# Kernel tuning notes

Measured on AMD Instinct MI355X. Metric: run time of the kernel, lower is better.

Reference implementation:

```python
import jax, jax.numpy as jnp
import numpy as np

L, V, D, H, F, S = 6, 32000, 768, 12, 3072, 1024
B, T = 2, 1024
DK = D // H
EPS = 1e-5  # torch LayerNorm default


def _ln(x, w, b):
    m = x.mean(-1, keepdims=True)
    v = ((x - m) ** 2).mean(-1, keepdims=True)
    return (x - m) / jnp.sqrt(v + EPS) * w + b


def setup_inputs() -> dict:
    key = jax.random.key(0)
    ks = jax.random.split(key, 16)
    n = lambda k, shape: jax.random.normal(k, shape, jnp.float32) * 0.02
    return {
        "x": jax.random.randint(ks[0], (B, T), 0, V),
        "tok_emb": n(ks[1], (V, D)),
        "pos_emb": n(ks[2], (S, D)),
        "ln1_w": jnp.ones((L, D), jnp.float32), "ln1_b": jnp.zeros((L, D), jnp.float32),
        "wq": n(ks[3], (L, D, D)), "bq": jnp.zeros((L, D), jnp.float32),
        "wk": n(ks[4], (L, D, D)), "bk": jnp.zeros((L, D), jnp.float32),
        "wv": n(ks[5], (L, D, D)), "bv": jnp.zeros((L, D), jnp.float32),
        "wo": n(ks[6], (L, D, D)), "bo": jnp.zeros((L, D), jnp.float32),
        "ln2_w": jnp.ones((L, D), jnp.float32), "ln2_b": jnp.zeros((L, D), jnp.float32),
        "w1": n(ks[7], (L, F, D)), "b1": jnp.zeros((L, F), jnp.float32),
        "w2": n(ks[8], (L, D, F)), "b2": jnp.zeros((L, D), jnp.float32),
        "lnf_w": jnp.ones((D,), jnp.float32), "lnf_b": jnp.zeros((D,), jnp.float32),
        "head_w": n(ks[9], (V, D)),
    }


def reference(x, tok_emb, pos_emb, ln1_w, ln1_b, wq, bq, wk, bk, wv, bv, wo, bo,
              ln2_w, ln2_b, w1, b1, w2, b2, lnf_w, lnf_b, head_w):
    Bx, Tx = x.shape
    h = tok_emb[x] + pos_emb[:Tx]                     # [B,T,D]
    causal = jnp.triu(jnp.ones((Tx, Tx), bool), 1)    # True above diagonal
    scale = 1.0 / np.sqrt(DK)
    for i in range(L):
        a = _ln(h, ln1_w[i], ln1_b[i])
        q = (a @ wq[i].T + bq[i]).reshape(Bx, Tx, H, DK).transpose(0, 2, 1, 3)
        k = (a @ wk[i].T + bk[i]).reshape(Bx, Tx, H, DK).transpose(0, 2, 1, 3)
        v = (a @ wv[i].T + bv[i]).reshape(Bx, Tx, H, DK).transpose(0, 2, 1, 3)
        scores = jnp.einsum("bhtd,bhsd->bhts", q, k) * scale  # [B,H,T,T]
        scores = jnp.where(causal, -jnp.inf, scores)
        attn = jax.nn.softmax(scores, axis=-1)
        ctx = jnp.einsum("bhts,bhsd->bhtd", attn, v)
        ctx = ctx.transpose(0, 2, 1, 3).reshape(Bx, Tx, D)
        h = h + ctx @ wo[i].T + bo[i]
        f = _ln(h, ln2_w[i], ln2_b[i])
        h = h + jax.nn.relu(f @ w1[i].T + b1[i]) @ w2[i].T + b2[i]
    h = _ln(h, lnf_w, lnf_b)
    return h @ head_w.T                               # [B,T,V] logits
```

## Files before the change

### kernel.cpp

```cpp
#include <hip/hip_runtime.h>

typedef unsigned short u16;
typedef __bf16 bf16x8 __attribute__((ext_vector_type(8)));
typedef float f32x4 __attribute__((ext_vector_type(4)));
typedef float f32x4v __attribute__((ext_vector_type(4)));
typedef u16 u16x4 __attribute__((ext_vector_type(4)));

__device__ __forceinline__ float bf2f(u16 u) {
    unsigned x = ((unsigned)u) << 16;
    return __builtin_bit_cast(float, x);
}
__device__ __forceinline__ u16 f2bf(float f) {
    unsigned x = __builtin_bit_cast(unsigned, f);
    unsigned r = (x + 0x7FFFu + ((x >> 16) & 1u)) >> 16;
    return (u16)r;
}

__global__ __launch_bounds__(256) void cvt_kernel(const float* __restrict__ in,
                                                  u16* __restrict__ out, long n) {
    for (long i = (long)blockIdx.x * 1024 + (long)threadIdx.x * 4; i < n;
         i += (long)gridDim.x * 1024) {
        f32x4v v = *(const f32x4v*)(in + i);
        u16x4 o;
        o.x = f2bf(v.x); o.y = f2bf(v.y); o.z = f2bf(v.z); o.w = f2bf(v.w);
        *(u16x4*)(out + i) = o;
    }
}

__global__ __launch_bounds__(256) void bias_fuse_kernel(const float* __restrict__ bq,
                                                        const float* __restrict__ bk,
                                                        const float* __restrict__ bv,
                                                        float* __restrict__ dst) {
    int i = blockIdx.x * 256 + threadIdx.x;
    if (i < 6 * 768) {
        int l = i / 768, j = i % 768;
        dst[l * 2304 + j] = bq[i];
        dst[l * 2304 + 768 + j] = bk[i];
        dst[l * 2304 + 1536 + j] = bv[i];
    }
}

__global__ __launch_bounds__(256) void embed_kernel(const int* __restrict__ x,
                                                    const float* __restrict__ tok,
                                                    const float* __restrict__ pos,
                                                    float* __restrict__ h) {
    int row = blockIdx.x;
    int t = row & 1023;
    long id = x[row];
    const float* te = tok + id * 768L;
    const float* pe = pos + (long)t * 768L;
    float* o = h + (long)row * 768L;
    for (int d = threadIdx.x; d < 768; d += 256) o[d] = te[d] + pe[d];
}

__global__ __launch_bounds__(256) void ln_kernel(const float* __restrict__ x,
                                                 const float* __restrict__ w,
                                                 const float* __restrict__ b,
                                                 u16* __restrict__ out) {
    __shared__ float red[4];
    int row = blockIdx.x;
    const float* xr = x + (long)row * 768L;
    int tid = threadIdx.x, lane = tid & 63, wid = tid >> 6;
    float v0 = xr[tid], v1 = xr[tid + 256], v2 = xr[tid + 512];
    float s = v0 + v1 + v2;
    for (int o = 32; o; o >>= 1) s += __shfl_xor(s, o);
    if (lane == 0) red[wid] = s;
    __syncthreads();
    float mean = (red[0] + red[1] + red[2] + red[3]) * (1.f / 768.f);
    __syncthreads();
    float d0 = v0 - mean, d1 = v1 - mean, d2 = v2 - mean;
    float q = d0 * d0 + d1 * d1 + d2 * d2;
    for (int o = 32; o; o >>= 1) q += __shfl_xor(q, o);
    if (lane == 0) red[wid] = q;
    __syncthreads();
    float var = (red[0] + red[1] + red[2] + red[3]) * (1.f / 768.f);
    float rstd = rsqrtf(var + 1e-5f);
    u16* orow = out + (long)row * 768L;
    orow[tid]       = f2bf(d0 * rstd * w[tid]       + b[tid]);
    orow[tid + 256] = f2bf(d1 * rstd * w[tid + 256] + b[tid + 256]);
    orow[tid + 512] = f2bf(d2 * rstd * w[tid + 512] + b[tid + 512]);
}

__global__ __launch_bounds__(192) void redln_kernel(
    const float* __restrict__ part, long pstride, int S,
    const float* __restrict__ bias, float* __restrict__ h,
    const float* __restrict__ w, const float* __restrict__ b,
    u16* __restrict__ out) {
    __shared__ float red[3];
    int row = blockIdx.x;
    int tid = threadIdx.x, lane = tid & 63, wid = tid >> 6;
    long base = (long)row * 768 + tid * 4;
    f32x4v x = *(const f32x4v*)(h + base);
    f32x4v bb = *(const f32x4v*)(bias + tid * 4);
    x += bb;
    for (int s = 0; s < S; s++) x += *(const f32x4v*)(part + (long)s * pstride + base);
    *(f32x4v*)(h + base) = x;
    float s = x.x + x.y + x.z + x.w;
    for (int o = 32; o; o >>= 1) s += __shfl_xor(s, o);
    if (lane == 0) red[wid] = s;
    __syncthreads();
    float mean = (red[0] + red[1] + red[2]) * (1.f / 768.f);
    __syncthreads();
    f32x4v d = x - mean;
    float q = d.x * d.x + d.y * d.y + d.z * d.z + d.w * d.w;
    for (int o = 32; o; o >>= 1) q += __shfl_xor(q, o);
    if (lane == 0) red[wid] = q;
    __syncthreads();
    float var = (red[0] + red[1] + red[2]) * (1.f / 768.f);
    float rstd = rsqrtf(var + 1e-5f);
    f32x4v wv = *(const f32x4v*)(w + tid * 4);
    f32x4v bv = *(const f32x4v*)(b + tid * 4);
    u16x4 o;
    o.x = f2bf(d.x * rstd * wv.x + bv.x);
    o.y = f2bf(d.y * rstd * wv.y + bv.y);
    o.z = f2bf(d.z * rstd * wv.z + bv.z);
    o.w = f2bf(d.w * rstd * wv.w + bv.w);
    *(u16x4*)(out + base) = o;
}

__global__ __launch_bounds__(256) void flash_kernel(
    const u16* __restrict__ qkv,
    const u16* __restrict__ vT,
    u16* __restrict__ ctx) {
    int z = blockIdx.z;
    int zb = z / 12, zh = z - zb * 12;
    int qt = (int)gridDim.x - 1 - (int)blockIdx.x;
    int q0 = qt * 64;
    int tid = threadIdx.x, lane = tid & 63, wid = tid >> 6;
    int rA = lane & 15, sA = lane >> 4;

    const u16* Qbase = qkv + (long)zb * 1024 * 2304 + zh * 64;
    const u16* Kbase = Qbase + 768;
    const u16* Vbase = vT + (long)z * 64 * 1024;

    __shared__ u16 Ks[64 * 64];
    __shared__ u16 Vs[64 * 64];
    __shared__ u16 Ps[4][16 * 64];

    bf16x8 aq[2];
    {
        const u16* qrow = Qbase + (long)(q0 + wid * 16 + rA) * 2304;
        aq[0] = *(const bf16x8*)(qrow + sA * 8);
        aq[1] = *(const bf16x8*)(qrow + 32 + sA * 8);
    }

    float m[4], l[4];
    f32x4 acc_o[4];
#pragma unroll
    for (int j = 0; j < 4; j++) { m[j] = -1e30f; l[j] = 0.f; }
#pragma unroll
    for (int nf = 0; nf < 4; nf++) acc_o[nf] = 0.f;

    int grow0 = q0 + wid * 16 + sA * 4;
    int nkv = qt + 1;
    for (int t = 0; t < nkv; ++t) {
        int kv0 = t * 64;
#pragma unroll
        for (int c0 = 0; c0 < 512; c0 += 256) {
            int c = c0 + tid;
            int row = c >> 3, half = (c >> 2) & 1, sl = c & 3;
            int ks = sl ^ ((row >> 1) & 3);
            __builtin_amdgcn_global_load_lds(
                (const __attribute__((address_space(1))) unsigned*)(Kbase + (long)(kv0 + row) * 2304 + half * 32 + ks * 8),
                (__attribute__((address_space(3))) unsigned*)(Ks + c * 8), 16, 0, 0);
        }
#pragma unroll
        for (int c0 = 0; c0 < 512; c0 += 256) {
            int c = c0 + tid;
            int row = c >> 3, half = (c >> 2) & 1, sl = c & 3;
            int ks = sl ^ ((row >> 1) & 3);
            __builtin_amdgcn_global_load_lds(
                (const __attribute__((address_space(1))) unsigned*)(Vbase + (long)row * 1024 + kv0 + half * 32 + ks * 8),
                (__attribute__((address_space(3))) unsigned*)(Vs + c * 8), 16, 0, 0);
        }
        __syncthreads();

        f32x4 s[4];
#pragma unroll
        for (int nf = 0; nf < 4; nf++) s[nf] = 0.f;
        __builtin_amdgcn_s_setprio(1);
#pragma unroll
        for (int h = 0; h < 2; h++)
#pragma unroll
            for (int nf = 0; nf < 4; nf++) {
                int row = nf * 16 + rA;
                bf16x8 bk_ = *(const bf16x8*)(Ks + row * 64 + h * 32 + ((sA ^ ((row >> 1) & 3))) * 8);
                s[nf] = __builtin_amdgcn_mfma_f32_16x16x32_bf16(aq[h], bk_, s[nf], 0, 0, 0);
            }
        __builtin_amdgcn_s_setprio(0);
#pragma unroll
        for (int nf = 0; nf < 4; nf++) {
            int col = kv0 + nf * 16 + rA;
#pragma unroll
            for (int j = 0; j < 4; j++)
                s[nf][j] = (col <= grow0 + j) ? s[nf][j] * 0.125f : -1e30f;
        }
        float pm[4];
#pragma unroll
        for (int j = 0; j < 4; j++) {
            float v = fmaxf(fmaxf(s[0][j], s[1][j]), fmaxf(s[2][j], s[3][j]));
#pragma unroll
            for (int o = 1; o < 16; o <<= 1) v = fmaxf(v, __shfl_xor(v, o));
            pm[j] = v;
        }
        float esc[4];
#pragma unroll
        for (int j = 0; j < 4; j++) {
            float mn = fmaxf(m[j], pm[j]);
            esc[j] = __expf(m[j] - mn);
            m[j] = mn;
        }
        float ts[4] = {0.f, 0.f, 0.f, 0.f};
#pragma unroll
        for (int nf = 0; nf < 4; nf++) {
            int c = nf * 16 + rA;
            int half = c >> 5, ch = (c >> 3) & 3, e = c & 7;
#pragma unroll
            for (int j = 0; j < 4; j++) {
                float p = __expf(s[nf][j] - m[j]);
                ts[j] += p;
                int r = sA * 4 + j;
                Ps[wid][r * 64 + half * 32 + (ch ^ ((r >> 1) & 3)) * 8 + e] = f2bf(p);
            }
        }
#pragma unroll
        for (int j = 0; j < 4; j++) {
            float v = ts[j];
#pragma unroll
            for (int o = 1; o < 16; o <<= 1) v += __shfl_xor(v, o);
            l[j] = l[j] * esc[j] + v;
        }
#pragma unroll
        for (int nf = 0; nf < 4; nf++)
#pragma unroll
            for (int j = 0; j < 4; j++) acc_o[nf][j] *= esc[j];

        __builtin_amdgcn_s_setprio(1);
#pragma unroll
        for (int h = 0; h < 2; h++) {
            bf16x8 ap = *(const bf16x8*)(Ps[wid] + rA * 64 + h * 32 + ((sA ^ ((rA >> 1) & 3))) * 8);
#pragma unroll
            for (int nf = 0; nf < 4; nf++) {
                int row = nf * 16 + rA;
                bf16x8 bv_ = *(const bf16x8*)(Vs + row * 64 + h * 32 + ((sA ^ ((row >> 1) & 3))) * 8);
                acc_o[nf] = __builtin_amdgcn_mfma_f32_16x16x32_bf16(ap, bv_, acc_o[nf], 0, 0, 0);
            }
        }
        __builtin_amdgcn_s_setprio(0);
        __syncthreads();
    }

    float inv[4];
#pragma unroll
    for (int j = 0; j < 4; j++) inv[j] = 1.f / l[j];
    u16* crow = ctx + ((long)zb * 1024 + q0 + wid * 16) * 768 + zh * 64;
#pragma unroll
    for (int nf = 0; nf < 4; nf++)
#pragma unroll
        for (int j = 0; j < 4; j++)
            crow[(long)(sA * 4 + j) * 768 + nf * 16 + rA] = f2bf(acc_o[nf][j] * inv[j]);
}

template <int BM, int BN, int BK, int EPI, int SK>
__global__ __launch_bounds__(256) void gemm8_kernel(
    const u16* __restrict__ A, int lda,
    const u16* __restrict__ Bm, int ldb,
    void* __restrict__ Cv, int ldc,
    const float* __restrict__ bias, int Kslice, int gm,
    u16* __restrict__ aux, int gemmBlocks, long partStride,
    const float* __restrict__ c0src, u16* __restrict__ c0dst, long c0n,
    const float* __restrict__ c1src, u16* __restrict__ c1dst, long c1n) {
    constexpr int CPR = BK / 8;
    constexpr int KH = BK / 32;
    int flat = blockIdx.x;
    int tid = threadIdx.x;
    if (flat >= gemmBlocks) {
        int P = (int)gridDim.x - gemmBlocks;
        int pid = flat - gemmBlocks;
        int P0 = P >> 1;
        const float* src; u16* dst; long n; long b0; long nb;
        if (pid < P0) { src = c0src; dst = c0dst; n = c0n; b0 = pid; nb = P0; }
        else { src = c1src; dst = c1dst; n = c1n; b0 = pid - P0; nb = P - P0; }
        if (src) {
            for (long i = b0 * 1024 + (long)tid * 4; i < n; i += nb * 1024) {
                f32x4v v = *(const f32x4v*)(src + i);
                u16x4 o;
                o.x = f2bf(v.x); o.y = f2bf(v.y); o.z = f2bf(v.z); o.w = f2bf(v.w);
                *(u16x4*)(dst + i) = o;
            }
        }
        return;
    }
    int nwg = gemmBlocks;
    int qq = nwg >> 3, rr = nwg & 7;
    int xcd = flat & 7, wi = flat >> 3;
    int swz = (xcd < rr) ? (xcd * (qq + 1) + wi) : (rr * (qq + 1) + (xcd - rr) * qq + wi);
    int slice = 0, wblk = swz;
    if (SK > 1) { int nbs = nwg / SK; slice = swz / nbs; wblk = swz - slice * nbs; }
    int ntile = wblk / gm, mt = wblk - ntile * gm;
    int bm0 = mt * BM, bn0 = ntile * BN;
    long koff = (long)slice * Kslice;
    const u16* Ab = A + (long)bm0 * lda + koff;
    const u16* Bb = Bm + (long)bn0 * ldb + koff;

    __shared__ u16 As[2][BM * BK];
    __shared__ u16 Bs[2][BN * BK];

    int lane = tid & 63, wid = tid >> 6;
    constexpr int WM = BM / 2, WN = BN / 2, MR = WM / 16, NR = WN / 16;
    int wm0 = (wid >> 1) * WM, wn0 = (wid & 1) * WN;

    f32x4 acc[MR][NR];
#pragma unroll
    for (int mi = 0; mi < MR; mi++)
#pragma unroll
        for (int ni = 0; ni < NR; ni++) acc[mi][ni] = 0.f;

    int nt = Kslice / BK;

    auto key = [](int row) { return (BK == 32) ? ((row >> 1) & 3) : (row & 7); };

    auto stage = [&](int buf, int k0) {
        constexpr int CA = BM * CPR;
#pragma unroll
        for (int c0 = 0; c0 < CA; c0 += 256) {
            int c = c0 + tid;
            int row = c / CPR, sl = c & (CPR - 1);
            int ks = sl ^ key(row);
            __builtin_amdgcn_global_load_lds(
                (const __attribute__((address_space(1))) unsigned*)(Ab + (long)row * lda + k0 + ks * 8),
                (__attribute__((address_space(3))) unsigned*)(As[buf] + c * 8), 16, 0, 0);
        }
        constexpr int CB = BN * CPR;
#pragma unroll
        for (int c0 = 0; c0 < CB; c0 += 256) {
            int c = c0 + tid;
            int row = c / CPR, sl = c & (CPR - 1);
            int ks = sl ^ key(row);
            __builtin_amdgcn_global_load_lds(
                (const __attribute__((address_space(1))) unsigned*)(Bb + (long)row * ldb + k0 + ks * 8),
                (__attribute__((address_space(3))) unsigned*)(Bs[buf] + c * 8), 16, 0, 0);
        }
    };

    stage(0, 0);
    __syncthreads();
    int cur = 0;
    int rA = lane & 15, sA = lane >> 4;
    for (int t = 0; t < nt; ++t) {
        if (t + 1 < nt) stage(cur ^ 1, (t + 1) * BK);
        bf16x8 af[MR][KH], bfr[NR][KH];
#pragma unroll
        for (int mi = 0; mi < MR; mi++) {
            int row = wm0 + mi * 16 + rA;
#pragma unroll
            for (int h = 0; h < KH; h++)
                af[mi][h] = *(const bf16x8*)(As[cur] + row * BK + (((h << 2) + sA) ^ key(row)) * 8);
        }
#pragma unroll
        for (int ni = 0; ni < NR; ni++) {
            int row = wn0 + ni * 16 + rA;
#pragma unroll
            for (int h = 0; h < KH; h++)
                bfr[ni][h] = *(const bf16x8*)(Bs[cur] + row * BK + (((h << 2) + sA) ^ key(row)) * 8);
        }
#pragma unroll
        for (int h = 0; h < KH; h++)
#pragma unroll
            for (int mi = 0; mi < MR; mi++)
#pragma unroll
                for (int ni = 0; ni < NR; ni++)
                    acc[mi][ni] = __builtin_amdgcn_mfma_f32_16x16x32_bf16(
                        af[mi][h], bfr[ni][h], acc[mi][ni], 0, 0, 0);
        __syncthreads();
        cur ^= 1;
    }

#pragma unroll
    for (int mi = 0; mi < MR; mi++)
#pragma unroll
        for (int ni = 0; ni < NR; ni++) {
            int gmb = bm0 + wm0 + mi * 16 + ((lane >> 4) << 2);
            int gn = bn0 + wn0 + ni * 16 + (lane & 15);
            if (EPI == 6) {
                if (gn < 1536) {
#pragma unroll
                    for (int j = 0; j < 4; j++)
                        ((u16*)Cv)[(long)(gmb + j) * ldc + gn] =
                            f2bf(acc[mi][ni][j] + bias[gn]);
                } else {
                    u16x4 o;
#pragma unroll
                    for (int j = 0; j < 4; j++) o[j] = f2bf(acc[mi][ni][j] + bias[gn]);
                    int hh = (gn - 1536) >> 6, dk = gn & 63;
                    long off = ((long)((gmb >> 10) * 12 + hh) * 64 + dk) * 1024 + (gmb & 1023);
                    *(u16x4*)(aux + off) = o;
                }
            } else {
#pragma unroll
                for (int j = 0; j < 4; j++) {
                    float v = acc[mi][ni][j];
                    long idx = (long)(gmb + j) * ldc + gn;
                    if (EPI == 2) ((u16*)Cv)[idx] = f2bf(fmaxf(v + bias[gn], 0.f));
                    else ((float*)Cv)[(long)slice * partStride + idx] = v;
                }
            }
        }
}

extern "C" void kernel_launch(void* const* d_in, const int* in_sizes, int n_in,
                              void* d_out, int out_size, void* d_ws, size_t ws_size,
                              hipStream_t stream) {
    const int L = 6, D = 768, F = 3072, T = 1024, V = 32000;
    const int M = 2048;
    const int* x = (const int*)d_in[0];
    const float* tok = (const float*)d_in[1];
    const float* pos = (const float*)d_in[2];
    const float* ln1w = (const float*)d_in[3];
    const float* ln1b = (const float*)d_in[4];
    const float* wq = (const float*)d_in[5];
    const float* bq = (const float*)d_in[6];
    const float* wk = (const float*)d_in[7];
    const float* bk = (const float*)d_in[8];
    const float* wv = (const float*)d_in[9];
    const float* bv = (const float*)d_in[10];
    const float* wo = (const float*)d_in[11];
    const float* bo = (const float*)d_in[12];
    const float* ln2w = (const float*)d_in[13];
    const float* ln2b = (const float*)d_in[14];
    const float* w1 = (const float*)d_in[15];
    const float* b1 = (const float*)d_in[16];
    const float* w2 = (const float*)d_in[17];
    const float* b2 = (const float*)d_in[18];
    const float* lnfw = (const float*)d_in[19];
    const float* lnfb = (const float*)d_in[20];
    const float* headw = (const float*)d_in[21];

    char* p = (char*)d_ws;
    auto alloc = [&](size_t bytes) {
        char* r = p;
        p += (bytes + 255) & ~(size_t)255;
        return r;
    };
    const long DD = (long)D * D, FD = (long)F * D;
    const long PS = (long)M * D;
    const long HC = 2048000;
    u16* qkvw_b = (u16*)alloc(L * 3 * DD * 2);
    u16* wo_b = (u16*)alloc(L * DD * 2);
    u16* w1_b = (u16*)alloc(L * FD * 2);
    u16* w2_b = (u16*)alloc(L * FD * 2);
    u16* hw_b = (u16*)alloc((long)V * D * 2);
    float* qkvbias = (float*)alloc(L * 2304 * 4);
    float* h = (float*)alloc((long)M * D * 4);
    u16* a = (u16*)alloc((long)M * D * 2);
    u16* qkvb = (u16*)alloc((long)M * 2304 * 2);
    u16* vT = (u16*)alloc(24L * 64 * T * 2);
    u16* ctxb = (u16*)alloc((long)M * D * 2);
    u16* f1 = (u16*)alloc((long)M * F * 2);
    float* part = (float*)alloc(4L * PS * 4);

    auto cvt = [&](const float* src, u16* dst, long n) {
        long blocks = (n + 1023) / 1024;
        if (blocks > 4096) blocks = 4096;
        cvt_kernel<<<dim3((unsigned)blocks), 256, 0, stream>>>(src, dst, n);
    };
    cvt(wq, qkvw_b, DD);
    cvt(wk, qkvw_b + DD, DD);
    cvt(wv, qkvw_b + 2 * DD, DD);
    cvt(wo, wo_b, DD);
    cvt(w1, w1_b, FD);
    cvt(w2, w2_b, FD);
    bias_fuse_kernel<<<dim3(18), 256, 0, stream>>>(bq, bk, bv, qkvbias);
    embed_kernel<<<dim3(M), 256, 0, stream>>>(x, tok, pos, h);
    ln_kernel<<<dim3(M), 256, 0, stream>>>(h, ln1w, ln1b, a);

    for (int i = 0; i < L; i++) {
        int nx = i + 1;
        bool hn = nx < L;
        {
            int pg = hn ? 128 : 0;
            gemm8_kernel<64, 128, 64, 6, 1><<<dim3(576 + pg), 256, 0, stream>>>(
                a, D, qkvw_b + i * 3 * DD, D, qkvb, 2304, qkvbias + i * 2304,
                D, 32, vT, 576, 0,
                hn ? wq + nx * DD : nullptr, qkvw_b + nx * 3 * DD, DD,
                hn ? wk + nx * DD : nullptr, qkvw_b + nx * 3 * DD + DD, DD);
        }
        flash_kernel<<<dim3(16, 1, 24), 256, 0, stream>>>(qkvb, vT, ctxb);
        gemm8_kernel<64, 128, 64, 5, 2><<<dim3(384 + 128), 256, 0, stream>>>(
            ctxb, D, wo_b + i * DD, D, part, D, nullptr, 384, 32, nullptr,
            384, PS,
            hn ? wv + nx * DD : nullptr, qkvw_b + nx * 3 * DD + 2 * DD, DD,
            hn ? wo + nx * DD : nullptr, wo_b + nx * DD, DD);
        redln_kernel<<<dim3(M), 192, 0, stream>>>(
            part, PS, 2, bo + i * D, h, ln2w + i * D, ln2b + i * D, a);
        gemm8_kernel<64, 128, 64, 2, 1><<<dim3(768 + 128), 256, 0, stream>>>(
            a, D, w1_b + i * FD, D, f1, F, b1 + i * F, D, 32, nullptr, 768, 0,
            hn ? w1 + nx * FD : nullptr, w1_b + nx * FD, FD,
            headw + (2 * i) * HC, hw_b + (2 * i) * HC, HC);
        gemm8_kernel<64, 128, 64, 5, 4><<<dim3(768 + 128), 256, 0, stream>>>(
            f1, F, w2_b + i * FD, F, part, D, nullptr, 768, 32, nullptr,
            768, PS,
            hn ? w2 + nx * FD : nullptr, w2_b + nx * FD, FD,
            headw + (2 * i + 1) * HC, hw_b + (2 * i + 1) * HC, HC);
        redln_kernel<<<dim3(M), 192, 0, stream>>>(
            part, PS, 4, b2 + i * D, h,
            hn ? ln1w + nx * D : lnfw, hn ? ln1b + nx * D : lnfb, a);
    }
    gemm8_kernel<128, 128, 32, 5, 1><<<dim3(4000), 256, 0, stream>>>(
        a, D, hw_b, D, d_out, V, nullptr, D, 16, nullptr, 4000, 0,
        nullptr, nullptr, 0, nullptr, nullptr, 0);
}
```

Measured before the change: 1.082 ms.

## Convert all weights upfront instead of overlapping conversion with GEMM blocks

Drops the scheme that hid next-layer weight and head-weight fp32-to-bf16 conversion inside extra blocks of each GEMM launch. All layers' weights and the head matrix are now converted upfront by a few large strided cvt launches, and GEMM grids shrink to their pure compute size. Embedding and the first LayerNorm are fused into one kernel, saving a pass over h. This simplifies the GEMM kernel and launch count but serialises about 160 MB of conversion traffic before any compute instead of overlapping it.

Measured after the change: 979.3 us. -9.5%, faster.

```diff
diff --git a/kernel.cpp b/kernel.cpp
--- a/kernel.cpp
+++ b/kernel.cpp
@@ -17,13 +17,15 @@
 }
 
 __global__ __launch_bounds__(256) void cvt_kernel(const float* __restrict__ in,
-                                                  u16* __restrict__ out, long n) {
+                                                  u16* __restrict__ out, long n,
+                                                  long chunk, long stride) {
     for (long i = (long)blockIdx.x * 1024 + (long)threadIdx.x * 4; i < n;
          i += (long)gridDim.x * 1024) {
         f32x4v v = *(const f32x4v*)(in + i);
         u16x4 o;
         o.x = f2bf(v.x); o.y = f2bf(v.y); o.z = f2bf(v.z); o.w = f2bf(v.w);
-        *(u16x4*)(out + i) = o;
+        long c = i / chunk, rrem = i - c * chunk;
+        *(u16x4*)(out + c * stride + rrem) = o;
     }
 }
 
@@ -40,28 +42,23 @@
     }
 }
 
-__global__ __launch_bounds__(256) void embed_kernel(const int* __restrict__ x,
-                                                    const float* __restrict__ tok,
-                                                    const float* __restrict__ pos,
-                                                    float* __restrict__ h) {
+__global__ __launch_bounds__(256) void embed_ln_kernel(
+    const int* __restrict__ x, const float* __restrict__ tok,
+    const float* __restrict__ pos, float* __restrict__ h,
+    const float* __restrict__ w, const float* __restrict__ b,
+    u16* __restrict__ out) {
+    __shared__ float red[4];
     int row = blockIdx.x;
     int t = row & 1023;
     long id = x[row];
     const float* te = tok + id * 768L;
     const float* pe = pos + (long)t * 768L;
-    float* o = h + (long)row * 768L;
-    for (int d = threadIdx.x; d < 768; d += 256) o[d] = te[d] + pe[d];
-}
-
-__global__ __launch_bounds__(256) void ln_kernel(const float* __restrict__ x,
-                                                 const float* __restrict__ w,
-                                                 const float* __restrict__ b,
-                                                 u16* __restrict__ out) {
-    __shared__ float red[4];
-    int row = blockIdx.x;
-    const float* xr = x + (long)row * 768L;
+    float* hr = h + (long)row * 768L;
     int tid = threadIdx.x, lane = tid & 63, wid = tid >> 6;
-    float v0 = xr[tid], v1 = xr[tid + 256], v2 = xr[tid + 512];
+    float v0 = te[tid] + pe[tid];
+    float v1 = te[tid + 256] + pe[tid + 256];
+    float v2 = te[tid + 512] + pe[tid + 512];
+    hr[tid] = v0; hr[tid + 256] = v1; hr[tid + 512] = v2;
     float s = v0 + v1 + v2;
     for (int o = 32; o; o >>= 1) s += __shfl_xor(s, o);
     if (lane == 0) red[wid] = s;
@@ -267,31 +264,12 @@
     const u16* __restrict__ Bm, int ldb,
     void* __restrict__ Cv, int ldc,
     const float* __restrict__ bias, int Kslice, int gm,
-    u16* __restrict__ aux, int gemmBlocks, long partStride,
-    const float* __restrict__ c0src, u16* __restrict__ c0dst, long c0n,
-    const float* __restrict__ c1src, u16* __restrict__ c1dst, long c1n) {
+    u16* __restrict__ aux, long partStride) {
     constexpr int CPR = BK / 8;
     constexpr int KH = BK / 32;
     int flat = blockIdx.x;
     int tid = threadIdx.x;
-    if (flat >= gemmBlocks) {
-        int P = (int)gridDim.x - gemmBlocks;
-        int pid = flat - gemmBlocks;
-        int P0 = P >> 1;
-        const float* src; u16* dst; long n; long b0; long nb;
-        if (pid < P0) { src = c0src; dst = c0dst; n = c0n; b0 = pid; nb = P0; }
-        else { src = c1src; dst = c1dst; n = c1n; b0 = pid - P0; nb = P - P0; }
-        if (src) {
-            for (long i = b0 * 1024 + (long)tid * 4; i < n; i += nb * 1024) {
-                f32x4v v = *(const f32x4v*)(src + i);
-                u16x4 o;
-                o.x = f2bf(v.x); o.y = f2bf(v.y); o.z = f2bf(v.z); o.w = f2bf(v.w);
-                *(u16x4*)(dst + i) = o;
-            }
-        }
-        return;
-    }
-    int nwg = gemmBlocks;
+    int nwg = gridDim.x;
     int qq = nwg >> 3, rr = nwg & 7;
     int xcd = flat & 7, wi = flat >> 3;
     int swz = (xcd < rr) ? (xcd * (qq + 1) + wi) : (rr * (qq + 1) + (xcd - rr) * qq + wi);
@@ -444,7 +422,6 @@
     };
     const long DD = (long)D * D, FD = (long)F * D;
     const long PS = (long)M * D;
-    const long HC = 2048000;
     u16* qkvw_b = (u16*)alloc(L * 3 * DD * 2);
     u16* wo_b = (u16*)alloc(L * DD * 2);
     u16* w1_b = (u16*)alloc(L * FD * 2);
@@ -459,54 +436,40 @@
     u16* f1 = (u16*)alloc((long)M * F * 2);
     float* part = (float*)alloc(4L * PS * 4);
 
-    auto cvt = [&](const float* src, u16* dst, long n) {
+    auto cvt = [&](const float* src, u16* dst, long n, long chunk, long stride) {
         long blocks = (n + 1023) / 1024;
         if (blocks > 4096) blocks = 4096;
-        cvt_kernel<<<dim3((unsigned)blocks), 256, 0, stream>>>(src, dst, n);
+        cvt_kernel<<<dim3((unsigned)blocks), 256, 0, stream>>>(src, dst, n, chunk, stride);
     };
-    cvt(wq, qkvw_b, DD);
-    cvt(wk, qkvw_b + DD, DD);
-    cvt(wv, qkvw_b + 2 * DD, DD);
-    cvt(wo, wo_b, DD);
-    cvt(w1, w1_b, FD);
-    cvt(w2, w2_b, FD);
+    cvt(wq, qkvw_b, L * DD, DD, 3 * DD);
+    cvt(wk, qkvw_b + DD, L * DD, DD, 3 * DD);
+    cvt(wv, qkvw_b + 2 * DD, L * DD, DD, 3 * DD);
+    cvt(wo, wo_b, L * DD, L * DD, L * DD);
+    cvt(w1, w1_b, L * FD, L * FD, L * FD);
+    cvt(w2, w2_b, L * FD, L * FD, L * FD);
+    cvt(headw, hw_b, (long)V * D, (long)V * D, (long)V * D);
     bias_fuse_kernel<<<dim3(18), 256, 0, stream>>>(bq, bk, bv, qkvbias);
-    embed_kernel<<<dim3(M), 256, 0, stream>>>(x, tok, pos, h);
-    ln_kernel<<<dim3(M), 256, 0, stream>>>(h, ln1w, ln1b, a);
+    embed_ln_kernel<<<dim3(M), 256, 0, stream>>>(x, tok, pos, h, ln1w, ln1b, a);
 
     for (int i = 0; i < L; i++) {
         int nx = i + 1;
         bool hn = nx < L;
-        {
-            int pg = hn ? 128 : 0;
-            gemm8_kernel<64, 128, 64, 6, 1><<<dim3(576 + pg), 256, 0, stream>>>(
-                a, D, qkvw_b + i * 3 * DD, D, qkvb, 2304, qkvbias + i * 2304,
-                D, 32, vT, 576, 0,
-                hn ? wq + nx * DD : nullptr, qkvw_b + nx * 3 * DD, DD,
-                hn ? wk + nx * DD : nullptr, qkvw_b + nx * 3 * DD + DD, DD);
-        }
+        gemm8_kernel<64, 128, 64, 6, 1><<<dim3(576), 256, 0, stream>>>(
+            a, D, qkvw_b + i * 3 * DD, D, qkvb, 2304, qkvbias + i * 2304,
+            D, 32, vT, 0);
         flash_kernel<<<dim3(16, 1, 24), 256, 0, stream>>>(qkvb, vT, ctxb);
-        gemm8_kernel<64, 128, 64, 5, 2><<<dim3(384 + 128), 256, 0, stream>>>(
-            ctxb, D, wo_b + i * DD, D, part, D, nullptr, 384, 32, nullptr,
-            384, PS,
-            hn ? wv + nx * DD : nullptr, qkvw_b + nx * 3 * DD + 2 * DD, DD,
-            hn ? wo + nx * DD : nullptr, wo_b + nx * DD, DD);
+        gemm8_kernel<64, 128, 64, 5, 2><<<dim3(384), 256, 0, stream>>>(
+            ctxb, D, wo_b + i * DD, D, part, D, nullptr, 384, 32, nullptr, PS);
         redln_kernel<<<dim3(M), 192, 0, stream>>>(
             part, PS, 2, bo + i * D, h, ln2w + i * D, ln2b + i * D, a);
-        gemm8_kernel<64, 128, 64, 2, 1><<<dim3(768 + 128), 256, 0, stream>>>(
-            a, D, w1_b + i * FD, D, f1, F, b1 + i * F, D, 32, nullptr, 768, 0,
-            hn ? w1 + nx * FD : nullptr, w1_b + nx * FD, FD,
-            headw + (2 * i) * HC, hw_b + (2 * i) * HC, HC);
-        gemm8_kernel<64, 128, 64, 5, 4><<<dim3(768 + 128), 256, 0, stream>>>(
-            f1, F, w2_b + i * FD, F, part, D, nullptr, 768, 32, nullptr,
-            768, PS,
-            hn ? w2 + nx * FD : nullptr, w2_b + nx * FD, FD,
-            headw + (2 * i + 1) * HC, hw_b + (2 * i + 1) * HC, HC);
+        gemm8_kernel<64, 128, 64, 2, 1><<<dim3(768), 256, 0, stream>>>(
+            a, D, w1_b + i * FD, D, f1, F, b1 + i * F, D, 32, nullptr, 0);
+        gemm8_kernel<64, 128, 64, 5, 4><<<dim3(768), 256, 0, stream>>>(
+            f1, F, w2_b + i * FD, F, part, D, nullptr, 768, 32, nullptr, PS);
         redln_kernel<<<dim3(M), 192, 0, stream>>>(
             part, PS, 4, b2 + i * D, h,
             hn ? ln1w + nx * D : lnfw, hn ? ln1b + nx * D : lnfb, a);
     }
     gemm8_kernel<128, 128, 32, 5, 1><<<dim3(4000), 256, 0, stream>>>(
-        a, D, hw_b, D, d_out, V, nullptr, D, 16, nullptr, 4000, 0,
-        nullptr, nullptr, 0, nullptr, nullptr, 0);
-}
+        a, D, hw_b, D, d_out, V, nullptr, D, 16, nullptr, 0);
+}
```
